# Optimization experiments

Measured on AMD Instinct MI355X. Metric: run time of the kernel, lower is better.

The kernel has to match this reference:

```python
import jax, jax.numpy as jnp
import numpy as np

H, W = 320, 320
HID = 64


def setup_inputs() -> dict:
    key = jax.random.key(0)
    k1, k2, k3 = jax.random.split(key, 3)
    K = jnp.array([[300.0, 0.0, 160.0], [0.0, 300.0, 160.0], [0.0, 0.0, 1.0]], jnp.float32)
    t_world_cam = jnp.array([[1.0, 0.0, 0.0, 0.0], [0.0, 1.0, 0.0, 0.0], [0.0, 0.0, 1.0, -2.5], [0.0, 0.0, 0.0, 1.0]], jnp.float32)
    return {
        'K': K,
        't_world_cam': t_world_cam,
        'aabb_min': -jnp.ones(3, jnp.float32),
        'aabb_max': jnp.ones(3, jnp.float32),
        'W1': jax.random.normal(k1, (3, HID), jnp.float32) * 0.5,
        'b1': jnp.zeros(HID, jnp.float32),
        'W2': jax.random.normal(k2, (HID, HID), jnp.float32) * (1.0 / np.sqrt(HID)),
        'b2': jnp.zeros(HID, jnp.float32),
        'W3': jax.random.normal(k3, (HID, 4), jnp.float32) * (1.0 / np.sqrt(HID)),
        'b3': jnp.zeros(4, jnp.float32),
        'n_samples': 32,
    }


def reference(K, t_world_cam, aabb_min, aabb_max, W1, b1, W2, b2, W3, b3, n_samples):
    dt = K.dtype
    # --- world rays (View.world_rays) ---
    fx, fy, cx, cy = K[0, 0], K[1, 1], K[0, 2], K[1, 2]
    u = jnp.arange(W, dtype=dt) + 0.5
    v = jnp.arange(H, dtype=dt) + 0.5
    vv, uu = jnp.meshgrid(v, u, indexing='ij')  # (H,W)
    d = jnp.stack([(uu - cx) / fx, (vv - cy) / fy, jnp.ones_like(uu)], -1)
    d = d / jnp.linalg.norm(d, axis=-1, keepdims=True)          # (H,W,3) view dirs
    R = t_world_cam[:3, :3]
    d = d.reshape(-1, 3) @ R.T                                   # (N,3) world dirs
    o = jnp.broadcast_to(t_world_cam[:3, 3], d.shape)            # (N,3) world origins
    # --- ray/AABB slab intersection ---
    inv = 1.0 / d
    t1 = (aabb_min - o) * inv
    t2 = (aabb_max - o) * inv
    tnear = jnp.max(jnp.minimum(t1, t2), -1)
    tfar = jnp.min(jnp.maximum(t1, t2), -1)
    hit = tnear < tfar
    tn = jnp.where(hit, tnear, 0.0)
    tf = jnp.where(hit, tfar, 1.0)
    # --- uniform sampling along rays ---
    frac = (jnp.arange(n_samples, dtype=dt) + 0.5) / n_samples
    ts = tn[:, None] + (tf - tn)[:, None] * frac                 # (N,S)
    xyz = o[:, None] + ts[..., None] * d[:, None]                # (N,S,3)
    nxyz = (xyz - aabb_min) / (aabb_max - aabb_min) * 2.0 - 1.0  # normalize to [-1,1]
    # --- radiance field MLP ---
    h = jax.nn.relu(nxyz @ W1 + b1)
    h = jax.nn.relu(h @ W2 + b2)
    raw = h @ W3 + b3                                            # (N,S,4)
    sigma = jax.nn.softplus(raw[..., 0])                         # (N,S)
    color = jax.nn.sigmoid(raw[..., 1:])                         # (N,S,3)
    # --- integrate_path: volumetric alpha compositing ---
    delta = jnp.concatenate([jnp.diff(ts, axis=-1), tf[:, None] - ts[:, -1:]], -1)
    sa = sigma * delta
    sa_cum = jnp.cumsum(sa, -1)
    T_prev = jnp.exp(-(sa_cum - sa))                             # transmittance before sample
    weights = T_prev * (1.0 - jnp.exp(-sa))
    rgb = jnp.einsum('ns,nsc->nc', weights, color)               # (N,3)
    alpha = 1.0 - jnp.exp(-sa_cum[:, -1])                        # 1 - T at ray exit
    rgb = jnp.where(hit[:, None], rgb, 0.0)
    alpha = jnp.where(hit, alpha, 0.0)
    img = jnp.concatenate([rgb, alpha[:, None]], -1).reshape(H, W, 4)
    return jnp.transpose(img, (2, 0, 1))                         # (4,H,W)
```

## Files before the change

### kernel.cpp

```cpp
#include <hip/hip_runtime.h>
#include <hip/hip_bf16.h>

#define IMG_H 320
#define IMG_W 320
#define NPIX (IMG_H * IMG_W)
#define HID 64
#define NS 32

typedef __attribute__((ext_vector_type(8))) short short8;
typedef __attribute__((ext_vector_type(4))) float float4v;
typedef __attribute__((ext_vector_type(4))) int   int4v;

#define W2T_OFF 0
#define W1T_OFF 4096
#define W3T_OFF (4096 + 2048)
#define B3P_FLT 3584
#define B2_FLT  3600
#define WS_BYTES 15360
#define PREP_BLOCKS 8

__device__ __forceinline__ unsigned f2bf(float f) {
    __hip_bfloat16 b = __float2bfloat16(f);
    return (unsigned)*reinterpret_cast<unsigned short*>(&b);
}

__device__ __forceinline__ unsigned cvtpk(float lo, float hi) {
    unsigned r;
    asm("v_cvt_pk_bf16_f32 %0, %1, %2" : "=v"(r) : "v"(lo), "v"(hi));
    return r;
}

__device__ __forceinline__ short8 packfrag(float4v lo, float4v hi) {
    int4v p;
    p[0] = (int)cvtpk(fmaxf(lo[0], 0.f), fmaxf(lo[1], 0.f));
    p[1] = (int)cvtpk(fmaxf(lo[2], 0.f), fmaxf(lo[3], 0.f));
    p[2] = (int)cvtpk(fmaxf(hi[0], 0.f), fmaxf(hi[1], 0.f));
    p[3] = (int)cvtpk(fmaxf(hi[2], 0.f), fmaxf(hi[3], 0.f));
    return *reinterpret_cast<short8*>(&p);
}

template <int CTRL, int RMASK>
__device__ __forceinline__ float dppadd(float x) {
    int s = __builtin_amdgcn_update_dpp(0, __float_as_int(x), CTRL, RMASK, 0xF, true);
    return x + __int_as_float(s);
}
__device__ __forceinline__ float scan32(float x) {
    x = dppadd<0x111, 0xF>(x);
    x = dppadd<0x112, 0xF>(x);
    x = dppadd<0x114, 0xF>(x);
    x = dppadd<0x118, 0xF>(x);
    x = dppadd<0x142, 0xA>(x);
    return x;
}

__device__ __forceinline__ void gload_lds16(const void* g, void* l) {
    __builtin_amdgcn_global_load_lds(
        (const __attribute__((address_space(1))) unsigned int*)g,
        (__attribute__((address_space(3))) unsigned int*)l, 16, 0, 0);
}

__global__ __launch_bounds__(256) void prep(const float* __restrict__ W1,
                                            const float* __restrict__ b1,
                                            const float* __restrict__ W2,
                                            const float* __restrict__ W3,
                                            const float* __restrict__ b3,
                                            const float* __restrict__ b2,
                                            short* __restrict__ wsS) {
    int t = blockIdx.x * 256 + threadIdx.x;
    const int STR = 256 * PREP_BLOCKS;
    float* wsF = reinterpret_cast<float*>(wsS);
    for (int i = t; i < 4096; i += STR) {
        int idx = i >> 9, m = (i >> 5) & 15, k2 = i & 31;
        int j3 = 32 * (idx >> 2) + 8 * (m >> 2) + 4 * ((idx >> 1) & 1) + (m & 3);
        int k  = 32 * (idx & 1) + k2;
        wsS[W2T_OFF + i] = (short)f2bf(W2[k * HID + j3]);
    }
    for (int i = t; i < 2048; i += STR) {
        int tt = i >> 9, m = (i >> 5) & 15, k = i & 31;
        int j = 32 * (tt >> 1) + 8 * (m >> 2) + 4 * (tt & 1) + (m & 3);
        float v = (k < 3) ? W1[k * HID + j] : ((k == 3) ? b1[j] : 0.0f);
        wsS[W1T_OFF + i] = (short)f2bf(v);
    }
    for (int i = t; i < 1024; i += STR) {
        int c = i >> 6, j = i & 63;
        float v = (c < 4) ? W3[j * 4 + c] : 0.0f;
        wsS[W3T_OFF + i] = (short)f2bf(v);
    }
    if (t < 16) wsF[B3P_FLT + t] = (t < 4) ? b3[t] : 0.0f;
    else if (t >= 16 && t < 80) wsF[B2_FLT + (t - 16)] = b2[t - 16];
    for (int i = t; i < (WS_BYTES / 4) - (B2_FLT + 64); i += STR)
        wsF[B2_FLT + 64 + i] = 0.0f;
}

__global__ __launch_bounds__(256) __attribute__((amdgpu_waves_per_eu(3, 3)))
void nerf_reg3(
    const float* __restrict__ Kmat, const float* __restrict__ Twc,
    const float* __restrict__ aabb_min, const float* __restrict__ aabb_max,
    const short* __restrict__ ws, float* __restrict__ out) {
    __shared__ __align__(16) short wlds[WS_BYTES / 2];
    __shared__ __align__(16) float pp[8][12];
    __shared__ __align__(16) float rawLds[4][256];

    const int tid  = threadIdx.x;
    const int wave = tid >> 6;
    const int lane = tid & 63;
    const int l15  = lane & 15;
    const int g    = lane >> 4;

    {
        const char* wsb = (const char*)ws;
        char* wl = (char*)wlds;
        for (int c = wave; c < WS_BYTES / 1024; c += 4)
            gload_lds16(wsb + c * 1024 + lane * 16, wl + c * 1024);
    }

    if (tid < 8) {
        int p = blockIdx.x * 8 + tid;
        int y = p / IMG_W, x = p - y * IMG_W;
        float fx = Kmat[0], cx = Kmat[2], fy = Kmat[4], cy = Kmat[5];
        float u = (float)x + 0.5f, v = (float)y + 0.5f;
        float dcx = (u - cx) * __builtin_amdgcn_rcpf(fx);
        float dcy = (v - cy) * __builtin_amdgcn_rcpf(fy);
        float dcz = 1.0f;
        float inorm = rsqrtf(dcx * dcx + dcy * dcy + dcz * dcz);
        dcx *= inorm; dcy *= inorm; dcz *= inorm;
        float dx = Twc[0] * dcx + Twc[1] * dcy + Twc[2]  * dcz;
        float dy = Twc[4] * dcx + Twc[5] * dcy + Twc[6]  * dcz;
        float dz = Twc[8] * dcx + Twc[9] * dcy + Twc[10] * dcz;
        float ox = Twc[3], oy = Twc[7], oz = Twc[11];

        float mnx = aabb_min[0], mny = aabb_min[1], mnz = aabb_min[2];
        float mxx = aabb_max[0], mxy = aabb_max[1], mxz = aabb_max[2];
        float ivx = __builtin_amdgcn_rcpf(dx);
        float ivy = __builtin_amdgcn_rcpf(dy);
        float ivz = __builtin_amdgcn_rcpf(dz);
        float t1x = (mnx - ox) * ivx, t2x = (mxx - ox) * ivx;
        float t1y = (mny - oy) * ivy, t2y = (mxy - oy) * ivy;
        float t1z = (mnz - oz) * ivz, t2z = (mxz - oz) * ivz;
        float tnear = fmaxf(fmaxf(fminf(t1x, t2x), fminf(t1y, t2y)), fminf(t1z, t2z));
        float tfar  = fminf(fminf(fmaxf(t1x, t2x), fmaxf(t1y, t2y)), fmaxf(t1z, t2z));
        bool hit = tnear < tfar;
        float tn = hit ? tnear : 0.0f;
        float tf = hit ? tfar  : 1.0f;
        float step = (tf - tn) * (1.0f / NS);
        float iex = 2.0f * __builtin_amdgcn_rcpf(mxx - mnx);
        float iey = 2.0f * __builtin_amdgcn_rcpf(mxy - mny);
        float iez = 2.0f * __builtin_amdgcn_rcpf(mxz - mnz);
        pp[tid][0] = dx * iex;
        pp[tid][1] = dy * iey;
        pp[tid][2] = dz * iez;
        pp[tid][3] = (ox - mnx) * iex - 1.0f;
        pp[tid][4] = (oy - mny) * iey - 1.0f;
        pp[tid][5] = (oz - mnz) * iez - 1.0f;
        pp[tid][6] = tn;
        pp[tid][7] = step;
        pp[tid][8] = hit ? 1.0f : 0.0f;
    }
    __syncthreads();

    const short* w2l = wlds + W2T_OFF;
    const short* w1l = wlds + W1T_OFF;
    const short* w3l = wlds + W3T_OFF;
    const float* bpf = reinterpret_cast<const float*>(wlds);
    float* rawf = rawLds[wave];

    const int s  = tid & 31;
    const int lp = (tid >> 5) & 7;

    float4v P0 = *reinterpret_cast<const float4v*>(&pp[lp][0]);
    float4v P1 = *reinterpret_cast<const float4v*>(&pp[lp][4]);
    float hitf = pp[lp][8];
    float step = P1[3];
    float tsv  = fmaf(step, (float)s + 0.5f, P1[2]);
    float nx = fmaf(tsv, P0[0], P0[3]);
    float ny = fmaf(tsv, P0[1], P1[0]);
    float nz = fmaf(tsv, P0[2], P1[1]);

    unsigned pd0 = cvtpk(nx, ny);
    unsigned pd1 = cvtpk(nz, 1.0f);

    short8 a1[4];
#pragma unroll
    for (int t = 0; t < 4; ++t)
        a1[t] = *reinterpret_cast<const short8*>(w1l + (t * 16 + l15) * 32 + 8 * g);
    short8 a2[8];
#pragma unroll
    for (int i = 0; i < 8; ++i)
        a2[i] = *reinterpret_cast<const short8*>(w2l + (i * 16 + l15) * 32 + 8 * g);
    short8 a3[2];
#pragma unroll
    for (int T3 = 0; T3 < 2; ++T3)
        a3[T3] = *reinterpret_cast<const short8*>(w3l + l15 * HID + 32 * T3 + 8 * g);
    float4v binit[4];
#pragma unroll
    for (int uu = 0; uu < 4; ++uu)
        binit[uu] = *reinterpret_cast<const float4v*>(
            bpf + B2_FLT + 32 * (uu >> 1) + 4 * (uu & 1) + 8 * g);
    float4v ci = *reinterpret_cast<const float4v*>(bpf + B3P_FLT + 4 * g);

    int u0v[4], u1v[4];
#pragma unroll
    for (int nt = 0; nt < 4; ++nt) {
        u0v[nt] = __shfl((int)pd0, 16 * nt + l15, 64);
        u1v[nt] = __shfl((int)pd1, 16 * nt + l15, 64);
    }

#pragma unroll
    for (int nt = 0; nt < 4; ++nt) {
        int4v bi;
        bi[0] = (g == 0) ? u0v[nt] : 0;
        bi[1] = (g == 0) ? u1v[nt] : 0;
        bi[2] = 0; bi[3] = 0;
        short8 bx = *reinterpret_cast<short8*>(&bi);

        float4v c1[4];
#pragma unroll
        for (int t = 0; t < 4; ++t)
            c1[t] = __builtin_amdgcn_mfma_f32_16x16x32_bf16(
                a1[t], bx, (float4v){0.f, 0.f, 0.f, 0.f}, 0, 0, 0);
        short8 pa0 = packfrag(c1[0], c1[1]);
        short8 pa1 = packfrag(c1[2], c1[3]);

        float4v c2[4];
#pragma unroll
        for (int uu = 0; uu < 4; ++uu) c2[uu] = binit[uu];
#pragma unroll
        for (int uu = 0; uu < 4; ++uu)
            c2[uu] = __builtin_amdgcn_mfma_f32_16x16x32_bf16(a2[uu * 2 + 0], pa0,
                                                             c2[uu], 0, 0, 0);
#pragma unroll
        for (int uu = 0; uu < 4; ++uu)
            c2[uu] = __builtin_amdgcn_mfma_f32_16x16x32_bf16(a2[uu * 2 + 1], pa1,
                                                             c2[uu], 0, 0, 0);
        short8 pb0 = packfrag(c2[0], c2[1]);
        short8 pb1 = packfrag(c2[2], c2[3]);

        float4v dv = __builtin_amdgcn_mfma_f32_16x16x32_bf16(a3[0], pb0, ci, 0, 0, 0);
        dv = __builtin_amdgcn_mfma_f32_16x16x32_bf16(a3[1], pb1, dv, 0, 0, 0);
        if (g == 0)
            *reinterpret_cast<float4v*>(rawf + (16 * nt + l15) * 4) = dv;
    }
    asm volatile("s_waitcnt lgkmcnt(0)" ::: "memory");

    float4v raw = *reinterpret_cast<const float4v*>(rawf + lane * 4);
    float r0 = raw[0], r1 = raw[1], r2 = raw[2], r3 = raw[3];

    float sigma = fmaxf(r0, 0.0f) + __logf(1.0f + __expf(-fabsf(r0)));
    float c0 = __builtin_amdgcn_rcpf(1.0f + __expf(-r1));
    float c1 = __builtin_amdgcn_rcpf(1.0f + __expf(-r2));
    float c2 = __builtin_amdgcn_rcpf(1.0f + __expf(-r3));
    float delta = (s == NS - 1) ? 0.5f * step : step;
    float sa = sigma * delta;

    float cum = scan32(sa);
    float Tprev = __expf(-(cum - sa));
    float w = Tprev * (1.0f - __expf(-sa));
    float rr = scan32(w * c0);
    float rg = scan32(w * c1);
    float rb = scan32(w * c2);

    if (s == NS - 1) {
        int pix = blockIdx.x * 8 + lp;
        float alpha = 1.0f - __expf(-cum);
        float o0 = rr, o1 = rg, o2 = rb;
        if (hitf == 0.0f) { o0 = 0.0f; o1 = 0.0f; o2 = 0.0f; alpha = 0.0f; }
        out[0 * NPIX + pix] = o0;
        out[1 * NPIX + pix] = o1;
        out[2 * NPIX + pix] = o2;
        out[3 * NPIX + pix] = alpha;
    }
}

extern "C" void kernel_launch(void* const* d_in, const int* in_sizes, int n_in,
                              void* d_out, int out_size, void* d_ws, size_t ws_size,
                              hipStream_t stream) {
    const float* Kmat = (const float*)d_in[0];
    const float* Twc  = (const float*)d_in[1];
    const float* amn  = (const float*)d_in[2];
    const float* amx  = (const float*)d_in[3];
    const float* W1   = (const float*)d_in[4];
    const float* b1   = (const float*)d_in[5];
    const float* W2   = (const float*)d_in[6];
    const float* b2   = (const float*)d_in[7];
    const float* W3   = (const float*)d_in[8];
    const float* b3   = (const float*)d_in[9];
    float* out = (float*)d_out;
    short* ws  = (short*)d_ws;

    prep<<<PREP_BLOCKS, 256, 0, stream>>>(W1, b1, W2, W3, b3, b2, ws);

    int blocks = NPIX * NS / 256;
    nerf_reg3<<<blocks, 256, 0, stream>>>(Kmat, Twc, amn, amx, ws, out);
}
```

Before: 74.82 us.

## Process four pixel groups per block and redistribute MLP output via replicated W3 rows

Each block now handles 32 pixels over four loop iterations, so the LDS weight load and the fragment loads into registers are amortized across four times more work and the grid shrinks by four. W3 is replicated across all 16 output rows, so every lane group receives the raw outputs directly from the MFMA result. This removes the rawLds round trip and its waitcnt, and per-lane selects pick the right tile instead. The launch bound moves from a fixed three waves per EU to a min-blocks hint of 2, which changes register pressure and occupancy. The inner loop is not unrolled, so per-block latency becomes serial across iterations.

```diff
diff --git a/kernel.cpp b/kernel.cpp
--- a/kernel.cpp
+++ b/kernel.cpp
@@ -6,6 +6,7 @@
 #define NPIX (IMG_H * IMG_W)
 #define HID 64
 #define NS 32
+#define ITER 4
 
 typedef __attribute__((ext_vector_type(8))) short short8;
 typedef __attribute__((ext_vector_type(4))) float float4v;
@@ -83,8 +84,7 @@
     }
     for (int i = t; i < 1024; i += STR) {
         int c = i >> 6, j = i & 63;
-        float v = (c < 4) ? W3[j * 4 + c] : 0.0f;
-        wsS[W3T_OFF + i] = (short)f2bf(v);
+        wsS[W3T_OFF + i] = (short)f2bf(W3[j * 4 + (c & 3)]);
     }
     if (t < 16) wsF[B3P_FLT + t] = (t < 4) ? b3[t] : 0.0f;
     else if (t >= 16 && t < 80) wsF[B2_FLT + (t - 16)] = b2[t - 16];
@@ -92,14 +92,12 @@
         wsF[B2_FLT + 64 + i] = 0.0f;
 }
 
-__global__ __launch_bounds__(256) __attribute__((amdgpu_waves_per_eu(3, 3)))
-void nerf_reg3(
+__global__ __launch_bounds__(256, 2) void nerf_reg5(
     const float* __restrict__ Kmat, const float* __restrict__ Twc,
     const float* __restrict__ aabb_min, const float* __restrict__ aabb_max,
     const short* __restrict__ ws, float* __restrict__ out) {
     __shared__ __align__(16) short wlds[WS_BYTES / 2];
-    __shared__ __align__(16) float pp[8][12];
-    __shared__ __align__(16) float rawLds[4][256];
+    __shared__ __align__(16) float pp[32][12];
 
     const int tid  = threadIdx.x;
     const int wave = tid >> 6;
@@ -114,8 +112,8 @@
             gload_lds16(wsb + c * 1024 + lane * 16, wl + c * 1024);
     }
 
-    if (tid < 8) {
-        int p = blockIdx.x * 8 + tid;
+    if (tid < 32) {
+        int p = blockIdx.x * 32 + tid;
         int y = p / IMG_W, x = p - y * IMG_W;
         float fx = Kmat[0], cx = Kmat[2], fy = Kmat[4], cy = Kmat[5];
         float u = (float)x + 0.5f, v = (float)y + 0.5f;
@@ -162,22 +160,10 @@
     const short* w1l = wlds + W1T_OFF;
     const short* w3l = wlds + W3T_OFF;
     const float* bpf = reinterpret_cast<const float*>(wlds);
-    float* rawf = rawLds[wave];
-
-    const int s  = tid & 31;
-    const int lp = (tid >> 5) & 7;
-
-    float4v P0 = *reinterpret_cast<const float4v*>(&pp[lp][0]);
-    float4v P1 = *reinterpret_cast<const float4v*>(&pp[lp][4]);
-    float hitf = pp[lp][8];
-    float step = P1[3];
-    float tsv  = fmaf(step, (float)s + 0.5f, P1[2]);
-    float nx = fmaf(tsv, P0[0], P0[3]);
-    float ny = fmaf(tsv, P0[1], P1[0]);
-    float nz = fmaf(tsv, P0[2], P1[1]);
-
-    unsigned pd0 = cvtpk(nx, ny);
-    unsigned pd1 = cvtpk(nz, 1.0f);
+
+    const int s   = tid & 31;
+    const int lp0 = (tid >> 5) & 7;
+    const float sph = (float)s + 0.5f;
 
     short8 a1[4];
 #pragma unroll
@@ -196,78 +182,95 @@
     for (int uu = 0; uu < 4; ++uu)
         binit[uu] = *reinterpret_cast<const float4v*>(
             bpf + B2_FLT + 32 * (uu >> 1) + 4 * (uu & 1) + 8 * g);
-    float4v ci = *reinterpret_cast<const float4v*>(bpf + B3P_FLT + 4 * g);
-
-    int u0v[4], u1v[4];
-#pragma unroll
-    for (int nt = 0; nt < 4; ++nt) {
-        u0v[nt] = __shfl((int)pd0, 16 * nt + l15, 64);
-        u1v[nt] = __shfl((int)pd1, 16 * nt + l15, 64);
-    }
-
-#pragma unroll
-    for (int nt = 0; nt < 4; ++nt) {
-        int4v bi;
-        bi[0] = (g == 0) ? u0v[nt] : 0;
-        bi[1] = (g == 0) ? u1v[nt] : 0;
-        bi[2] = 0; bi[3] = 0;
-        short8 bx = *reinterpret_cast<short8*>(&bi);
-
-        float4v c1[4];
-#pragma unroll
-        for (int t = 0; t < 4; ++t)
-            c1[t] = __builtin_amdgcn_mfma_f32_16x16x32_bf16(
-                a1[t], bx, (float4v){0.f, 0.f, 0.f, 0.f}, 0, 0, 0);
-        short8 pa0 = packfrag(c1[0], c1[1]);
-        short8 pa1 = packfrag(c1[2], c1[3]);
-
-        float4v c2[4];
-#pragma unroll
-        for (int uu = 0; uu < 4; ++uu) c2[uu] = binit[uu];
-#pragma unroll
-        for (int uu = 0; uu < 4; ++uu)
-            c2[uu] = __builtin_amdgcn_mfma_f32_16x16x32_bf16(a2[uu * 2 + 0], pa0,
-                                                             c2[uu], 0, 0, 0);
-#pragma unroll
-        for (int uu = 0; uu < 4; ++uu)
-            c2[uu] = __builtin_amdgcn_mfma_f32_16x16x32_bf16(a2[uu * 2 + 1], pa1,
-                                                             c2[uu], 0, 0, 0);
-        short8 pb0 = packfrag(c2[0], c2[1]);
-        short8 pb1 = packfrag(c2[2], c2[3]);
-
-        float4v dv = __builtin_amdgcn_mfma_f32_16x16x32_bf16(a3[0], pb0, ci, 0, 0, 0);
-        dv = __builtin_amdgcn_mfma_f32_16x16x32_bf16(a3[1], pb1, dv, 0, 0, 0);
-        if (g == 0)
-            *reinterpret_cast<float4v*>(rawf + (16 * nt + l15) * 4) = dv;
-    }
-    asm volatile("s_waitcnt lgkmcnt(0)" ::: "memory");
-
-    float4v raw = *reinterpret_cast<const float4v*>(rawf + lane * 4);
-    float r0 = raw[0], r1 = raw[1], r2 = raw[2], r3 = raw[3];
-
-    float sigma = fmaxf(r0, 0.0f) + __logf(1.0f + __expf(-fabsf(r0)));
-    float c0 = __builtin_amdgcn_rcpf(1.0f + __expf(-r1));
-    float c1 = __builtin_amdgcn_rcpf(1.0f + __expf(-r2));
-    float c2 = __builtin_amdgcn_rcpf(1.0f + __expf(-r3));
-    float delta = (s == NS - 1) ? 0.5f * step : step;
-    float sa = sigma * delta;
-
-    float cum = scan32(sa);
-    float Tprev = __expf(-(cum - sa));
-    float w = Tprev * (1.0f - __expf(-sa));
-    float rr = scan32(w * c0);
-    float rg = scan32(w * c1);
-    float rb = scan32(w * c2);
-
-    if (s == NS - 1) {
-        int pix = blockIdx.x * 8 + lp;
-        float alpha = 1.0f - __expf(-cum);
-        float o0 = rr, o1 = rg, o2 = rb;
-        if (hitf == 0.0f) { o0 = 0.0f; o1 = 0.0f; o2 = 0.0f; alpha = 0.0f; }
-        out[0 * NPIX + pix] = o0;
-        out[1 * NPIX + pix] = o1;
-        out[2 * NPIX + pix] = o2;
-        out[3 * NPIX + pix] = alpha;
+    float4v ci = *reinterpret_cast<const float4v*>(bpf + B3P_FLT);
+
+#pragma unroll 1
+    for (int it = 0; it < ITER; ++it) {
+        const int lp = it * 8 + lp0;
+
+        float4v P0 = *reinterpret_cast<const float4v*>(&pp[lp][0]);
+        float4v P1 = *reinterpret_cast<const float4v*>(&pp[lp][4]);
+        float hitf = pp[lp][8];
+        float step = P1[3];
+        float tsv  = fmaf(step, sph, P1[2]);
+        float nx = fmaf(tsv, P0[0], P0[3]);
+        float ny = fmaf(tsv, P0[1], P1[0]);
+        float nz = fmaf(tsv, P0[2], P1[1]);
+
+        unsigned pd0 = cvtpk(nx, ny);
+        unsigned pd1 = cvtpk(nz, 1.0f);
+
+        int u0v[4], u1v[4];
+#pragma unroll
+        for (int nt = 0; nt < 4; ++nt) {
+            u0v[nt] = __shfl((int)pd0, 16 * nt + l15, 64);
+            u1v[nt] = __shfl((int)pd1, 16 * nt + l15, 64);
+        }
+
+        float4v dvs[4];
+#pragma unroll
+        for (int nt = 0; nt < 4; ++nt) {
+            int4v bi;
+            bi[0] = (g == 0) ? u0v[nt] : 0;
+            bi[1] = (g == 0) ? u1v[nt] : 0;
+            bi[2] = 0; bi[3] = 0;
+            short8 bx = *reinterpret_cast<short8*>(&bi);
+
+            float4v c1[4];
+#pragma unroll
+            for (int t = 0; t < 4; ++t)
+                c1[t] = __builtin_amdgcn_mfma_f32_16x16x32_bf16(
+                    a1[t], bx, (float4v){0.f, 0.f, 0.f, 0.f}, 0, 0, 0);
+            short8 pa0 = packfrag(c1[0], c1[1]);
+            short8 pa1 = packfrag(c1[2], c1[3]);
+
+            float4v c2[4];
+#pragma unroll
+            for (int uu = 0; uu < 4; ++uu) c2[uu] = binit[uu];
+#pragma unroll
+            for (int uu = 0; uu < 4; ++uu)
+                c2[uu] = __builtin_amdgcn_mfma_f32_16x16x32_bf16(a2[uu * 2 + 0], pa0,
+                                                                 c2[uu], 0, 0, 0);
+#pragma unroll
+            for (int uu = 0; uu < 4; ++uu)
+                c2[uu] = __builtin_amdgcn_mfma_f32_16x16x32_bf16(a2[uu * 2 + 1], pa1,
+                                                                 c2[uu], 0, 0, 0);
+            short8 pb0 = packfrag(c2[0], c2[1]);
+            short8 pb1 = packfrag(c2[2], c2[3]);
+
+            float4v dv = __builtin_amdgcn_mfma_f32_16x16x32_bf16(a3[0], pb0, ci, 0, 0, 0);
+            dvs[nt] = __builtin_amdgcn_mfma_f32_16x16x32_bf16(a3[1], pb1, dv, 0, 0, 0);
+        }
+
+        float r0 = (g == 0) ? dvs[0][0] : (g == 1) ? dvs[1][0] : (g == 2) ? dvs[2][0] : dvs[3][0];
+        float r1 = (g == 0) ? dvs[0][1] : (g == 1) ? dvs[1][1] : (g == 2) ? dvs[2][1] : dvs[3][1];
+        float r2 = (g == 0) ? dvs[0][2] : (g == 1) ? dvs[1][2] : (g == 2) ? dvs[2][2] : dvs[3][2];
+        float r3 = (g == 0) ? dvs[0][3] : (g == 1) ? dvs[1][3] : (g == 2) ? dvs[2][3] : dvs[3][3];
+
+        float sigma = fmaxf(r0, 0.0f) + __logf(1.0f + __expf(-fabsf(r0)));
+        float c0 = __builtin_amdgcn_rcpf(1.0f + __expf(-r1));
+        float c1 = __builtin_amdgcn_rcpf(1.0f + __expf(-r2));
+        float c2 = __builtin_amdgcn_rcpf(1.0f + __expf(-r3));
+        float delta = (s == NS - 1) ? 0.5f * step : step;
+        float sa = sigma * delta;
+
+        float cum = scan32(sa);
+        float Tprev = __expf(-(cum - sa));
+        float w = Tprev * (1.0f - __expf(-sa));
+        float rr = scan32(w * c0);
+        float rg = scan32(w * c1);
+        float rb = scan32(w * c2);
+
+        if (s == NS - 1) {
+            int pix = blockIdx.x * 32 + lp;
+            float alpha = 1.0f - __expf(-cum);
+            float o0 = rr, o1 = rg, o2 = rb;
+            if (hitf == 0.0f) { o0 = 0.0f; o1 = 0.0f; o2 = 0.0f; alpha = 0.0f; }
+            out[0 * NPIX + pix] = o0;
+            out[1 * NPIX + pix] = o1;
+            out[2 * NPIX + pix] = o2;
+            out[3 * NPIX + pix] = alpha;
+        }
     }
 }
 
@@ -289,6 +292,6 @@
 
     prep<<<PREP_BLOCKS, 256, 0, stream>>>(W1, b1, W2, W3, b3, b2, ws);
 
-    int blocks = NPIX * NS / 256;
-    nerf_reg3<<<blocks, 256, 0, stream>>>(Kmat, Twc, amn, amx, ws, out);
-}
+    int blocks = NPIX * NS / 256 / ITER;
+    nerf_reg5<<<blocks, 256, 0, stream>>>(Kmat, Twc, amn, amx, ws, out);
+}
```

After: 65.16 us. -12.9%, faster.
